# Kernel optimization log

Measured on AMD Instinct MI355X. Metric: run time of the kernel, lower is better.

The kernel has to match this reference:

```python
import jax, jax.numpy as jnp
import numpy as np

H = 16          # num_attention_heads
GRID = 16       # crop_size // patch_size
TOK_PER_FRAME = GRID * GRID


def _rope(x, pos, dim):
    # x: (B,H,N,dim), pos: (N,) int positions
    half = dim // 2
    omega = jnp.arange(half, dtype=x.dtype) / (dim / 2.0)
    inv = 1.0 / (10000.0 ** omega)                      # (half,)
    freq = pos.astype(x.dtype)[:, None] * inv            # (N, half)
    sin = jnp.concatenate([jnp.sin(freq), jnp.sin(freq)], axis=-1)  # (N, dim)  (tile, per source)
    cos = jnp.concatenate([jnp.cos(freq), jnp.cos(freq)], axis=-1)
    y = x.reshape(*x.shape[:-1], half, 2)
    y1, y2 = y[..., 0], y[..., 1]
    rot = jnp.stack((-y2, y1), axis=-1).reshape(x.shape)  # interleaved rotate-pairs
    return x * cos + rot * sin


def _apply_3d_rope(qk, f_ids, h_ids, w_ids, d_dim):
    s = 0
    parts = []
    for pos in (f_ids, h_ids, w_ids):
        parts.append(_rope(qk[..., s:s + d_dim], pos, d_dim))
        s += d_dim
    if s < qk.shape[-1]:
        parts.append(qk[..., s:])
    return jnp.concatenate(parts, axis=-1)


def setup_inputs() -> dict:
    key = jax.random.key(0)
    ks = jax.random.split(key, 5)
    D = 1024
    B, N = 4, 2048
    sc = 0.02
    return {
        "hidden_states": jax.random.normal(ks[0], (B, N, D), jnp.float32),
        "Wq": jax.random.normal(ks[1], (D, D), jnp.float32) * sc,
        "bq": jnp.zeros((D,), jnp.float32),
        "Wk": jax.random.normal(ks[2], (D, D), jnp.float32) * sc,
        "bk": jnp.zeros((D,), jnp.float32),
        "Wv": jax.random.normal(ks[3], (D, D), jnp.float32) * sc,
        "bv": jnp.zeros((D,), jnp.float32),
        "Wo": jax.random.normal(ks[4], (D, D), jnp.float32) * sc,
        "bo": jnp.zeros((D,), jnp.float32),
    }


def reference(hidden_states, Wq, bq, Wk, bk, Wv, bv, Wo, bo):
    B, N, D = hidden_states.shape
    hd = D // H
    d_dim = 2 * (hd // 3 // 2)  # per-component rotary dim (20 for hd=64)

    def heads(x):  # (B,N,D) -> (B,H,N,hd)
        return x.reshape(B, N, H, hd).transpose(0, 2, 1, 3)

    q = heads(hidden_states @ Wq + bq)
    k = heads(hidden_states @ Wk + bk)
    v = heads(hidden_states @ Wv + bv)

    ids = jnp.arange(N)
    f_ids = ids // TOK_PER_FRAME
    rem = ids - TOK_PER_FRAME * f_ids
    h_ids = rem // GRID
    w_ids = rem - GRID * h_ids

    q = _apply_3d_rope(q, f_ids, h_ids, w_ids, d_dim)
    k = _apply_3d_rope(k, f_ids, h_ids, w_ids, d_dim)

    scale = hd ** -0.5
    attn = jnp.einsum('bhqd,bhkd->bhqk', q, k) * scale
    attn = jax.nn.softmax(attn.astype(jnp.float32), axis=-1).astype(q.dtype)
    ctx = jnp.einsum('bhqk,bhkd->bhqd', attn, v)
    ctx = ctx.transpose(0, 2, 1, 3).reshape(B, N, D)
    return ctx @ Wo + bo
```

## Files before the change

### kernel.cpp

```cpp
#include <hip/hip_runtime.h>
#include <stdint.h>

#define H_   16
#define NS_  2048
#define B_   4
#define DM_  1024
#define HD_  64
#define MTOT (B_*NS_)

typedef __attribute__((ext_vector_type(8)))  short bf16x8;
typedef __attribute__((ext_vector_type(4)))  float f32x4;
typedef __attribute__((ext_vector_type(16))) float f32x16;

__device__ __forceinline__ unsigned short f2bf(float f){
  union { float f; unsigned u; } v; v.f = f;
  unsigned r = v.u + 0x7FFFu + ((v.u >> 16) & 1u);
  return (unsigned short)(r >> 16);
}
__device__ __forceinline__ float bf2f(unsigned short u){
  union { unsigned u; float f; } v; v.u = ((unsigned)u) << 16;
  return v.f;
}
__device__ __forceinline__ unsigned pk2(float a, float b){
  return (unsigned)f2bf(a) | ((unsigned)f2bf(b) << 16);
}
__device__ __forceinline__ unsigned cvtpk(float a, float b){
  unsigned r;
  asm("v_cvt_pk_bf16_f32 %0, %1, %2" : "=v"(r) : "v"(a), "v"(b));
  return r;
}
__device__ __forceinline__ float exp2a(float x){
  float r;
  asm("v_exp_f32 %0, %1" : "=v"(r) : "v"(x));
  return r;
}
__device__ __forceinline__ void gll16(const void* g, void* l){
  __builtin_amdgcn_global_load_lds(
      (const __attribute__((address_space(1))) unsigned int*)g,
      (__attribute__((address_space(3))) unsigned int*)l,
      16, 0, 0);
}

__global__ void k_cast_x(const float* __restrict__ x, unsigned short* __restrict__ xb){
  long i = ((long)blockIdx.x*256 + threadIdx.x)*4;
  float4 v = *(const float4*)(x + i);
  ushort4 o; o.x=f2bf(v.x); o.y=f2bf(v.y); o.z=f2bf(v.z); o.w=f2bf(v.w);
  *(ushort4*)(xb + i) = o;
}

__global__ void k_wt4(const float* __restrict__ W0, const float* __restrict__ W1,
                      const float* __restrict__ W2, const float* __restrict__ W3,
                      unsigned short* __restrict__ T0, unsigned short* __restrict__ T1,
                      unsigned short* __restrict__ T2, unsigned short* __restrict__ T3){
  __shared__ float tile[64][65];
  const int z = blockIdx.z;
  const float* W = (z==0)? W0 : (z==1)? W1 : (z==2)? W2 : W3;
  unsigned short* Wt = (z==0)? T0 : (z==1)? T1 : (z==2)? T2 : T3;
  int kt = blockIdx.y*64, nt = blockIdx.x*64;
  int t = threadIdx.x;
  int r = t >> 4, c4 = (t & 15)*4;
#pragma unroll
  for (int i=0;i<4;i++){
    int k = r + i*16;
    float4 v = *(const float4*)(W + (size_t)(kt + k)*DM_ + nt + c4);
    tile[k][c4] = v.x; tile[k][c4+1]=v.y; tile[k][c4+2]=v.z; tile[k][c4+3]=v.w;
  }
  __syncthreads();
#pragma unroll
  for (int i=0;i<4;i++){
    int n = r + i*16;
    ushort4 o;
    o.x = f2bf(tile[c4+0][n]); o.y = f2bf(tile[c4+1][n]);
    o.z = f2bf(tile[c4+2][n]); o.w = f2bf(tile[c4+3][n]);
    *(ushort4*)(Wt + (size_t)(nt + n)*DM_ + kt + c4) = o;
  }
}

__global__ void k_tab(float2* __restrict__ tab){
  int n = blockIdx.x*64 + threadIdx.x;
  int f = n >> 8, rem = n & 255, hh = rem >> 4, ww = rem & 15;
  float pos[3]; pos[0]=(float)f; pos[1]=(float)hh; pos[2]=(float)ww;
#pragma unroll
  for (int c=0;c<3;c++)
#pragma unroll
    for (int i=0;i<10;i++){
      float inv = exp2f(-(float)i * 1.3287712379549449f);
      float s, co;
      sincosf(pos[c]*inv, &s, &co);
      tab[n*30 + c*10 + i] = make_float2(co, s);
    }
}

__device__ __forceinline__ void stage256(const unsigned short* __restrict__ gsrc,
                                         char* ldst, int tid){
  const int srow = tid >> 3;
  const int gch  = (tid & 7) ^ (srow & 7);
  const unsigned short* gp = gsrc + (size_t)srow*DM_ + gch*8;
  char* lp = ldst + tid*16;
#pragma unroll
  for (int j=0;j<4;j++)
    gll16(gp + (size_t)(j*64)*DM_, lp + j*8192);
}

template<int MODE>
__global__ __launch_bounds__(512, 2) void k_gemm256(
    const unsigned short* __restrict__ A,
    const unsigned short* __restrict__ w0,
    const unsigned short* __restrict__ w1,
    const unsigned short* __restrict__ w2,
    const float* __restrict__ b0,
    const float* __restrict__ b1,
    const float* __restrict__ b2,
    unsigned short* __restrict__ Qb,
    unsigned short* __restrict__ Kb,
    unsigned short* __restrict__ VTb,
    float* __restrict__ Fout)
{
  extern __shared__ char smem[];
  char* aL = smem;
  char* bL = smem + 65536;
  const int tid = threadIdx.x, lane = tid & 63, w = tid >> 6;
  const int qc = lane & 15, g = lane >> 4;
  const int wm = (w >> 2)*128, wn = (w & 3)*64;

  int mat, mt, nt;
  {
    int id = blockIdx.x;
    if (MODE == 0){
      int wg = (id & 7)*48 + (id >> 3);
      mat = wg >> 7; int rem = wg & 127;
      mt = (rem >> 2)*256; nt = (rem & 3)*256;
    } else {
      int wg = (id & 7)*16 + (id >> 3);
      mat = 0; mt = (wg >> 2)*256; nt = (wg & 3)*256;
    }
  }
  const unsigned short* Wt = (MODE==1)? w0 : ((mat==0)? w0 : (mat==1)? w1 : w2);
  const float* bias        = (MODE==1)? b0 : ((mat==0)? b0 : (mat==1)? b1 : b2);

  const unsigned short* Ab = A  + (size_t)mt*DM_;
  const unsigned short* Bb = Wt + (size_t)nt*DM_;

  stage256(Ab,      aL,         tid);
  stage256(Bb,      bL,         tid);
  stage256(Ab + 64, aL + 32768, tid);
  stage256(Bb + 64, bL + 32768, tid);

  f32x4 acc[8][4] = {};

  for (int kt = 0; kt < 16; ++kt){
    const int bu = kt & 1;
    if (kt < 15) asm volatile("s_waitcnt vmcnt(8)" ::: "memory");
    else         asm volatile("s_waitcnt vmcnt(0)" ::: "memory");
    __builtin_amdgcn_s_barrier();
    __builtin_amdgcn_sched_barrier(0);
    const char* aT = aL + bu*32768;
    const char* bT = bL + bu*32768;

    bf16x8 bfr[4][2], af[4][2], af2[4][2];
#pragma unroll
    for (int n=0;n<4;n++)
#pragma unroll
      for (int ks=0;ks<2;ks++){
        int row = wn + n*16 + qc;
        bfr[n][ks] = *(const bf16x8*)(bT + row*128 + ((ks*64 + g*16) ^ ((row&7)<<4)));
      }
#pragma unroll
    for (int m=0;m<4;m++)
#pragma unroll
      for (int ks=0;ks<2;ks++){
        int row = wm + m*16 + qc;
        af[m][ks] = *(const bf16x8*)(aT + row*128 + ((ks*64 + g*16) ^ ((row&7)<<4)));
      }
    __builtin_amdgcn_s_setprio(1);
#pragma unroll
    for (int m=0;m<4;m++)
#pragma unroll
      for (int n=0;n<4;n++)
#pragma unroll
        for (int ks=0;ks<2;ks++)
          acc[m][n] = __builtin_amdgcn_mfma_f32_16x16x32_bf16(af[m][ks], bfr[n][ks], acc[m][n], 0,0,0);
    __builtin_amdgcn_s_setprio(0);
#pragma unroll
    for (int m=0;m<4;m++)
#pragma unroll
      for (int ks=0;ks<2;ks++){
        int row = wm + 64 + m*16 + qc;
        af2[m][ks] = *(const bf16x8*)(aT + row*128 + ((ks*64 + g*16) ^ ((row&7)<<4)));
      }
    asm volatile("s_waitcnt lgkmcnt(0)" ::: "memory");
    __builtin_amdgcn_sched_barrier(0);
    __builtin_amdgcn_s_barrier();
    __builtin_amdgcn_sched_barrier(0);
    if (kt < 14){
      stage256(Ab + (size_t)(kt+2)*64, aL + bu*32768, tid);
      stage256(Bb + (size_t)(kt+2)*64, bL + bu*32768, tid);
    }
    __builtin_amdgcn_s_setprio(1);
#pragma unroll
    for (int m=0;m<4;m++)
#pragma unroll
      for (int n=0;n<4;n++)
#pragma unroll
        for (int ks=0;ks<2;ks++)
          acc[4+m][n] = __builtin_amdgcn_mfma_f32_16x16x32_bf16(af2[m][ks], bfr[n][ks], acc[4+m][n], 0,0,0);
    __builtin_amdgcn_s_setprio(0);
  }

  if (MODE == 1){
#pragma unroll
    for (int n=0;n<4;n++){
      int col = nt + wn + n*16 + qc;
      float bv = bias[col];
#pragma unroll
      for (int m=0;m<8;m++){
#pragma unroll
        for (int r=0;r<4;r++){
          int mrow = mt + wm + m*16 + g*4 + r;
          Fout[(size_t)mrow*DM_ + col] = acc[m][n][r] + bv;
        }
      }
    }
  } else if (mat < 2){
    unsigned short* out = (mat==0)? Qb : Kb;
#pragma unroll
    for (int n=0;n<4;n++){
      int col = nt + wn + n*16 + qc;
      float bv = bias[col];
      int hh = col >> 6, d = col & 63;
#pragma unroll
      for (int m=0;m<8;m++){
#pragma unroll
        for (int r=0;r<4;r++){
          int mrow = mt + wm + m*16 + g*4 + r;
          size_t idx = (((size_t)(mrow >> 11)*H_ + hh)*NS_ + (mrow & (NS_-1)))*HD_ + d;
          out[idx] = f2bf(acc[m][n][r] + bv);
        }
      }
    }
  } else {
#pragma unroll
    for (int n=0;n<4;n++){
      int col = nt + wn + n*16 + qc;
      float bv = bias[col];
      int hh = col >> 6, d = col & 63;
#pragma unroll
      for (int m=0;m<8;m++){
        int mrow0 = mt + wm + m*16 + g*4;
        int b = mrow0 >> 11, ntk = mrow0 & (NS_-1);
        int pos = (ntk & ~12) | ((ntk & 4) << 1) | ((ntk & 8) >> 1);
        ushort4 o;
        o.x = f2bf(acc[m][n][0] + bv);
        o.y = f2bf(acc[m][n][1] + bv);
        o.z = f2bf(acc[m][n][2] + bv);
        o.w = f2bf(acc[m][n][3] + bv);
        *(ushort4*)(VTb + (((size_t)(b*H_ + hh)*HD_ + d)*NS_ + pos)) = o;
      }
    }
  }
}

#define QSCALE 0.18033688011112042f
__global__ void k_rope(unsigned short* __restrict__ Qb, unsigned short* __restrict__ Kb,
                       const float2* __restrict__ tab)
{
  const int t = threadIdx.x;
  const int d4 = (t & 15)*4;
  const long gtok = (long)blockIdx.x*16 + (t >> 4);
  size_t base = (size_t)gtok*HD_ + d4;
  if (d4 >= 60){
    ushort4 v = *(ushort4*)(Qb + base);
    ushort4 o;
    o.x = f2bf(bf2f(v.x)*QSCALE); o.y = f2bf(bf2f(v.y)*QSCALE);
    o.z = f2bf(bf2f(v.z)*QSCALE); o.w = f2bf(bf2f(v.w)*QSCALE);
    *(ushort4*)(Qb + base) = o;
    return;
  }
  const int n = (int)(gtok & (NS_-1));
  const int c = d4 / 20;
  const int dd = d4 - c*20;
  const float2* tb = tab + n*30 + c*10;
  float2 cs0 = tb[(dd+0) % 10];
  float2 cs1 = tb[(dd+1) % 10];
  float2 cs2 = tb[(dd+2) % 10];
  float2 cs3 = tb[(dd+3) % 10];
#pragma unroll
  for (int which = 0; which < 2; which++){
    unsigned short* P = which ? Kb : Qb;
    float sc = which ? 1.f : QSCALE;
    ushort4 v = *(ushort4*)(P + base);
    float x0=bf2f(v.x), x1=bf2f(v.y), x2=bf2f(v.z), x3=bf2f(v.w);
    ushort4 o;
    o.x = f2bf((x0*cs0.x - x1*cs0.y)*sc);
    o.y = f2bf((x1*cs1.x + x0*cs1.y)*sc);
    o.z = f2bf((x2*cs2.x - x3*cs2.y)*sc);
    o.w = f2bf((x3*cs3.x + x2*cs3.y)*sc);
    *(ushort4*)(P + base) = o;
  }
}

__global__ __launch_bounds__(256, 4) void k_attn(const unsigned short* __restrict__ Q,
                                                 const unsigned short* __restrict__ K,
                                                 const unsigned short* __restrict__ VT,
                                                 unsigned short* __restrict__ ctxout)
{
  __shared__ __attribute__((aligned(16))) char smem[32768];
  const int tid  = threadIdx.x;
  const int lane = tid & 63, w = tid >> 6;
  const int qcol = lane & 31, h = lane >> 5;
  const int sw   = (lane & 7) << 4;
  const int bh   = blockIdx.x;
  const int q0   = blockIdx.y*128 + w*32;

  const unsigned short* Qp = Q  + ((size_t)bh*NS_ + q0)*HD_;
  const unsigned short* Kp = K  + (size_t)bh*NS_*HD_;
  const unsigned short* Vp = VT + (size_t)bh*HD_*NS_;

  const int trow = tid >> 3;
  const int tc   = (tid & 7) ^ (trow & 7);

  bf16x8 qf[4];
#pragma unroll
  for (int i=0;i<4;i++)
    qf[i] = *(const bf16x8*)(Qp + (size_t)qcol*HD_ + 16*i + 8*h);

  {
    const unsigned short* gk = Kp + (size_t)trow*HD_ + tc*8;
    const unsigned short* gv = Vp + (size_t)trow*NS_ + tc*8;
    gll16(gk,          smem + w*1024);
    gll16(gk + 32*HD_, smem + 4096 + w*1024);
    gll16(gv,          smem + 8192 + w*1024);
    gll16(gv + 32*NS_, smem + 8192 + 4096 + w*1024);
  }

  f32x16 ctx0 = {}, ctx1 = {};
  float mrun = -1e30f, lp = 0.f;

  for (int t = 0; t < NS_/64; ++t){
    const int curo = (t & 1) * 16384;
    __syncthreads();
    if (t + 1 < NS_/64){
      const int kb = (t+1)*64;
      const int nxt = ((t+1) & 1) * 16384;
      const unsigned short* gk = Kp + (size_t)(kb + trow)*HD_ + tc*8;
      const unsigned short* gv = Vp + (size_t)trow*NS_ + kb + tc*8;
      gll16(gk,          smem + nxt + w*1024);
      gll16(gk + 32*HD_, smem + nxt + 4096 + w*1024);
      gll16(gv,          smem + nxt + 8192 + w*1024);
      gll16(gv + 32*NS_, smem + nxt + 8192 + 4096 + w*1024);
    }
    const char* kls = smem + curo;
    const char* vls = smem + curo + 8192;

#pragma unroll
    for (int s = 0; s < 2; ++s){
      f32x16 st = {};
      __builtin_amdgcn_s_setprio(1);
#pragma unroll
      for (int i=0;i<4;i++){
        bf16x8 kf = *(const bf16x8*)(kls + ((((32*s + qcol)*128) + 32*i + 16*h) ^ sw));
        st = __builtin_amdgcn_mfma_f32_32x32x16_bf16(kf, qf[i], st, 0,0,0);
      }
      __builtin_amdgcn_s_setprio(0);
      float a0 = fmaxf(fmaxf(st[0],  st[1]),  st[2]);
      float a1 = fmaxf(fmaxf(st[3],  st[4]),  st[5]);
      float a2 = fmaxf(fmaxf(st[6],  st[7]),  st[8]);
      float a3 = fmaxf(fmaxf(st[9],  st[10]), st[11]);
      float a4 = fmaxf(fmaxf(st[12], st[13]), st[14]);
      float tm = fmaxf(fmaxf(fmaxf(a0,a1),a2), fmaxf(fmaxf(a3,a4),st[15]));
      if (!__all(tm - mrun <= 11.5f)){
        float tp = fmaxf(tm, __shfl_xor(tm, 32));
        float mnew = fmaxf(mrun, tp);
        float alpha = exp2a(mrun - mnew);
        lp *= alpha;
#pragma unroll
        for (int r=0;r<16;r++){ ctx0[r]*=alpha; ctx1[r]*=alpha; }
        mrun = mnew;
      }
      unsigned u[8];
      float ps = 0.f;
#pragma unroll
      for (int r=0;r<8;r++){
        float ea = exp2a(st[2*r]   - mrun);
        float eb = exp2a(st[2*r+1] - mrun);
        unsigned uu = cvtpk(ea, eb);
        u[r] = uu;
        union { unsigned q; float f; } lo, hi;
        lo.q = uu << 16; hi.q = uu & 0xFFFF0000u;
        ps += lo.f + hi.f;
      }
      lp += ps;
      bf16x8 pf0 = __builtin_bit_cast(bf16x8, make_uint4(u[0],u[1],u[2],u[3]));
      bf16x8 pf1 = __builtin_bit_cast(bf16x8, make_uint4(u[4],u[5],u[6],u[7]));

      __builtin_amdgcn_s_setprio(1);
#pragma unroll
      for (int kc=0; kc<2; ++kc){
        const bf16x8 pf = kc ? pf1 : pf0;
        bf16x8 vf0 = *(const bf16x8*)(vls + ((qcol)*128      + ((64*s + 32*kc + 16*h) ^ sw)));
        ctx0 = __builtin_amdgcn_mfma_f32_32x32x16_bf16(vf0, pf, ctx0, 0,0,0);
        bf16x8 vf1 = *(const bf16x8*)(vls + ((32 + qcol)*128 + ((64*s + 32*kc + 16*h) ^ sw)));
        ctx1 = __builtin_amdgcn_mfma_f32_32x32x16_bf16(vf1, pf, ctx1, 0,0,0);
      }
      __builtin_amdgcn_s_setprio(0);
    }
  }

  float lsum = lp + __shfl_xor(lp, 32);
  float linv = 1.f / lsum;
  __syncthreads();
  char* reg = smem + w*4096;
#pragma unroll
  for (int rq=0; rq<4; ++rq){
    int db0 = 8*rq + 4*h;
    uint2 v0, v1;
    v0.x = pk2(ctx0[4*rq+0]*linv, ctx0[4*rq+1]*linv);
    v0.y = pk2(ctx0[4*rq+2]*linv, ctx0[4*rq+3]*linv);
    v1.x = pk2(ctx1[4*rq+0]*linv, ctx1[4*rq+1]*linv);
    v1.y = pk2(ctx1[4*rq+2]*linv, ctx1[4*rq+3]*linv);
    *(uint2*)(reg + qcol*128 + db0*2)      = v0;
    *(uint2*)(reg + qcol*128 + (32+db0)*2) = v1;
  }
  __syncthreads();
  const int b = bh >> 4, head = bh & 15;
  unsigned short* outp = ctxout + ((size_t)b*NS_ + q0)*DM_ + head*HD_;
#pragma unroll
  for (int p=0;p<4;p++){
    int row = p*8 + (lane>>3);
    uint4 v = *(const uint4*)(reg + row*128 + (lane&7)*16);
    *(uint4*)(outp + (size_t)row*DM_ + (lane&7)*8) = v;
  }
}

extern "C" void kernel_launch(void* const* d_in, const int* in_sizes, int n_in,
                              void* d_out, int out_size, void* d_ws, size_t ws_size,
                              hipStream_t stream)
{
  const float* hs = (const float*)d_in[0];
  const float* Wq = (const float*)d_in[1];
  const float* bq = (const float*)d_in[2];
  const float* Wk = (const float*)d_in[3];
  const float* bk = (const float*)d_in[4];
  const float* Wv = (const float*)d_in[5];
  const float* bv = (const float*)d_in[6];
  const float* Wo = (const float*)d_in[7];
  const float* bo = (const float*)d_in[8];

  char* ws = (char*)d_ws;
  size_t off = 0;
  auto alloc = [&](size_t b){ void* p = ws + off; off += (b + 255) & ~(size_t)255; return p; };
  unsigned short* xb  = (unsigned short*)alloc((size_t)MTOT*DM_*2);
  unsigned short* wqt = (unsigned short*)alloc((size_t)DM_*DM_*2);
  unsigned short* wkt = (unsigned short*)alloc((size_t)DM_*DM_*2);
  unsigned short* wvt = (unsigned short*)alloc((size_t)DM_*DM_*2);
  unsigned short* wot = (unsigned short*)alloc((size_t)DM_*DM_*2);
  float2*         tab = (float2*)alloc((size_t)NS_*30*sizeof(float2));
  unsigned short* Qb  = (unsigned short*)alloc((size_t)MTOT*DM_*2);
  unsigned short* Kb  = (unsigned short*)alloc((size_t)MTOT*DM_*2);
  unsigned short* VTb = (unsigned short*)alloc((size_t)MTOT*DM_*2);
  unsigned short* cxb = (unsigned short*)alloc((size_t)MTOT*DM_*2);

  hipFuncSetAttribute((const void*)k_gemm256<0>,
                      hipFuncAttributeMaxDynamicSharedMemorySize, 131072);
  hipFuncSetAttribute((const void*)k_gemm256<1>,
                      hipFuncAttributeMaxDynamicSharedMemorySize, 131072);

  k_cast_x<<<dim3(MTOT*DM_/1024), dim3(256), 0, stream>>>(hs, xb);
  k_wt4<<<dim3(16,16,4), dim3(256), 0, stream>>>(Wq, Wk, Wv, Wo, wqt, wkt, wvt, wot);
  k_tab<<<dim3(32), dim3(64), 0, stream>>>(tab);

  k_gemm256<0><<<dim3(384), dim3(512), 131072, stream>>>(
      xb, wqt, wkt, wvt, bq, bk, bv, Qb, Kb, VTb, (float*)nullptr);

  k_rope<<<dim3(64*NS_/16), dim3(256), 0, stream>>>(Qb, Kb, tab);

  k_attn<<<dim3(64, 16), dim3(256), 0, stream>>>(Qb, Kb, VTb, cxb);

  k_gemm256<1><<<dim3(128), dim3(512), 131072, stream>>>(
      cxb, wot, nullptr, nullptr, bo, nullptr, nullptr,
      nullptr, nullptr, nullptr, (float*)d_out);
}
```

Baseline: 240.0 us.

## Merge prep kernels, store Q/K token-major, restructure rope and attention QK

Folds the x cast, weight transposes and rope-table kernels into a single launch with block-range dispatch, removing two launches. The QKV GEMM now writes Q and K in plain (B,N,D) row-major order instead of a head-major scatter, so the epilogue stores stay coalesced along columns. The rope kernel and the attention loads are updated for the row stride of DM_, and rope handles 8 elements per thread. In attention, both 32-row QK^T MFMA tiles are issued before the softmax to give the scheduler more overlap. In exchange, attention K loads become strided across rows of 1024 elements, which may hurt load efficiency.

```diff
diff --git a/kernel.cpp b/kernel.cpp
--- a/kernel.cpp
+++ b/kernel.cpp
@@ -41,54 +41,60 @@
       16, 0, 0);
 }
 
-__global__ void k_cast_x(const float* __restrict__ x, unsigned short* __restrict__ xb){
-  long i = ((long)blockIdx.x*256 + threadIdx.x)*4;
-  float4 v = *(const float4*)(x + i);
-  ushort4 o; o.x=f2bf(v.x); o.y=f2bf(v.y); o.z=f2bf(v.z); o.w=f2bf(v.w);
-  *(ushort4*)(xb + i) = o;
-}
-
-__global__ void k_wt4(const float* __restrict__ W0, const float* __restrict__ W1,
-                      const float* __restrict__ W2, const float* __restrict__ W3,
-                      unsigned short* __restrict__ T0, unsigned short* __restrict__ T1,
-                      unsigned short* __restrict__ T2, unsigned short* __restrict__ T3){
+__global__ void k_prep(const float* __restrict__ hs, unsigned short* __restrict__ xb,
+                       const float* __restrict__ W0, const float* __restrict__ W1,
+                       const float* __restrict__ W2, const float* __restrict__ W3,
+                       unsigned short* __restrict__ T0, unsigned short* __restrict__ T1,
+                       unsigned short* __restrict__ T2, unsigned short* __restrict__ T3,
+                       float2* __restrict__ tab)
+{
   __shared__ float tile[64][65];
-  const int z = blockIdx.z;
-  const float* W = (z==0)? W0 : (z==1)? W1 : (z==2)? W2 : W3;
-  unsigned short* Wt = (z==0)? T0 : (z==1)? T1 : (z==2)? T2 : T3;
-  int kt = blockIdx.y*64, nt = blockIdx.x*64;
-  int t = threadIdx.x;
-  int r = t >> 4, c4 = (t & 15)*4;
-#pragma unroll
-  for (int i=0;i<4;i++){
-    int k = r + i*16;
-    float4 v = *(const float4*)(W + (size_t)(kt + k)*DM_ + nt + c4);
-    tile[k][c4] = v.x; tile[k][c4+1]=v.y; tile[k][c4+2]=v.z; tile[k][c4+3]=v.w;
-  }
-  __syncthreads();
-#pragma unroll
-  for (int i=0;i<4;i++){
-    int n = r + i*16;
-    ushort4 o;
-    o.x = f2bf(tile[c4+0][n]); o.y = f2bf(tile[c4+1][n]);
-    o.z = f2bf(tile[c4+2][n]); o.w = f2bf(tile[c4+3][n]);
-    *(ushort4*)(Wt + (size_t)(nt + n)*DM_ + kt + c4) = o;
-  }
-}
-
-__global__ void k_tab(float2* __restrict__ tab){
-  int n = blockIdx.x*64 + threadIdx.x;
-  int f = n >> 8, rem = n & 255, hh = rem >> 4, ww = rem & 15;
-  float pos[3]; pos[0]=(float)f; pos[1]=(float)hh; pos[2]=(float)ww;
-#pragma unroll
-  for (int c=0;c<3;c++)
-#pragma unroll
-    for (int i=0;i<10;i++){
-      float inv = exp2f(-(float)i * 1.3287712379549449f);
-      float s, co;
-      sincosf(pos[c]*inv, &s, &co);
-      tab[n*30 + c*10 + i] = make_float2(co, s);
-    }
+  const int bid = blockIdx.x, t = threadIdx.x;
+  if (bid < 8192){
+    long i = ((long)bid*256 + t)*4;
+    float4 v = *(const float4*)(hs + i);
+    ushort4 o; o.x=f2bf(v.x); o.y=f2bf(v.y); o.z=f2bf(v.z); o.w=f2bf(v.w);
+    *(ushort4*)(xb + i) = o;
+    return;
+  }
+  if (bid < 9216){
+    int id = bid - 8192;
+    const int z = id >> 8; id &= 255;
+    const float* W = (z==0)? W0 : (z==1)? W1 : (z==2)? W2 : W3;
+    unsigned short* Wt = (z==0)? T0 : (z==1)? T1 : (z==2)? T2 : T3;
+    int kt = (id >> 4)*64, nt = (id & 15)*64;
+    int r = t >> 4, c4 = (t & 15)*4;
+#pragma unroll
+    for (int i=0;i<4;i++){
+      int k = r + i*16;
+      float4 v = *(const float4*)(W + (size_t)(kt + k)*DM_ + nt + c4);
+      tile[k][c4] = v.x; tile[k][c4+1]=v.y; tile[k][c4+2]=v.z; tile[k][c4+3]=v.w;
+    }
+    __syncthreads();
+#pragma unroll
+    for (int i=0;i<4;i++){
+      int n = r + i*16;
+      ushort4 o;
+      o.x = f2bf(tile[c4+0][n]); o.y = f2bf(tile[c4+1][n]);
+      o.z = f2bf(tile[c4+2][n]); o.w = f2bf(tile[c4+3][n]);
+      *(ushort4*)(Wt + (size_t)(nt + n)*DM_ + kt + c4) = o;
+    }
+    return;
+  }
+  {
+    int n = (bid - 9216)*256 + t;
+    int f = n >> 8, rem = n & 255, hh = rem >> 4, ww = rem & 15;
+    float pos[3]; pos[0]=(float)f; pos[1]=(float)hh; pos[2]=(float)ww;
+#pragma unroll
+    for (int c=0;c<3;c++)
+#pragma unroll
+      for (int i=0;i<10;i++){
+        float inv = exp2f(-(float)i * 1.3287712379549449f);
+        float s, co;
+        sincosf(pos[c]*inv, &s, &co);
+        tab[n*30 + c*10 + i] = make_float2(co, s);
+      }
+  }
 }
 
 __device__ __forceinline__ void stage256(const unsigned short* __restrict__ gsrc,
@@ -227,14 +233,12 @@
     for (int n=0;n<4;n++){
       int col = nt + wn + n*16 + qc;
       float bv = bias[col];
-      int hh = col >> 6, d = col & 63;
 #pragma unroll
       for (int m=0;m<8;m++){
 #pragma unroll
         for (int r=0;r<4;r++){
           int mrow = mt + wm + m*16 + g*4 + r;
-          size_t idx = (((size_t)(mrow >> 11)*H_ + hh)*NS_ + (mrow & (NS_-1)))*HD_ + d;
-          out[idx] = f2bf(acc[m][n][r] + bv);
+          out[(size_t)mrow*DM_ + col] = f2bf(acc[m][n][r] + bv);
         }
       }
     }
@@ -265,37 +269,38 @@
                        const float2* __restrict__ tab)
 {
   const int t = threadIdx.x;
-  const int d4 = (t & 15)*4;
-  const long gtok = (long)blockIdx.x*16 + (t >> 4);
-  size_t base = (size_t)gtok*HD_ + d4;
-  if (d4 >= 60){
-    ushort4 v = *(ushort4*)(Qb + base);
-    ushort4 o;
-    o.x = f2bf(bf2f(v.x)*QSCALE); o.y = f2bf(bf2f(v.y)*QSCALE);
-    o.z = f2bf(bf2f(v.z)*QSCALE); o.w = f2bf(bf2f(v.w)*QSCALE);
-    *(ushort4*)(Qb + base) = o;
-    return;
-  }
-  const int n = (int)(gtok & (NS_-1));
-  const int c = d4 / 20;
-  const int dd = d4 - c*20;
-  const float2* tb = tab + n*30 + c*10;
-  float2 cs0 = tb[(dd+0) % 10];
-  float2 cs1 = tb[(dd+1) % 10];
-  float2 cs2 = tb[(dd+2) % 10];
-  float2 cs3 = tb[(dd+3) % 10];
+  const long token = (long)blockIdx.x*2 + (t >> 7);
+  const int fd = (t & 127)*8;
+  const int n = (int)(token & (NS_-1));
+  const int d = fd & 63;
+  const float2* tb = tab + n*30;
+  float2 cs[8];
+#pragma unroll
+  for (int j=0;j<8;j++){
+    int e = d + j;
+    if (e < 60){
+      int c = e/20; int rr = e - 20*c; if (rr >= 10) rr -= 10;
+      cs[j] = tb[c*10 + rr];
+    } else cs[j] = make_float2(1.f, 0.f);
+  }
+  size_t base = (size_t)token*DM_ + fd;
 #pragma unroll
   for (int which = 0; which < 2; which++){
     unsigned short* P = which ? Kb : Qb;
     float sc = which ? 1.f : QSCALE;
-    ushort4 v = *(ushort4*)(P + base);
-    float x0=bf2f(v.x), x1=bf2f(v.y), x2=bf2f(v.z), x3=bf2f(v.w);
-    ushort4 o;
-    o.x = f2bf((x0*cs0.x - x1*cs0.y)*sc);
-    o.y = f2bf((x1*cs1.x + x0*cs1.y)*sc);
-    o.z = f2bf((x2*cs2.x - x3*cs2.y)*sc);
-    o.w = f2bf((x3*cs3.x + x2*cs3.y)*sc);
-    *(ushort4*)(P + base) = o;
+    ushort4 va = *(ushort4*)(P + base);
+    ushort4 vb = *(ushort4*)(P + base + 4);
+    float x[8] = {bf2f(va.x),bf2f(va.y),bf2f(va.z),bf2f(va.w),
+                  bf2f(vb.x),bf2f(vb.y),bf2f(vb.z),bf2f(vb.w)};
+    unsigned short o[8];
+#pragma unroll
+    for (int j=0;j<8;j+=2){
+      o[j]   = f2bf((x[j]*cs[j].x     - x[j+1]*cs[j].y)  *sc);
+      o[j+1] = f2bf((x[j+1]*cs[j+1].x + x[j]*cs[j+1].y)  *sc);
+    }
+    ushort4 oa = {o[0],o[1],o[2],o[3]}, ob = {o[4],o[5],o[6],o[7]};
+    *(ushort4*)(P + base)     = oa;
+    *(ushort4*)(P + base + 4) = ob;
   }
 }
 
@@ -310,10 +315,11 @@
   const int qcol = lane & 31, h = lane >> 5;
   const int sw   = (lane & 7) << 4;
   const int bh   = blockIdx.x;
+  const int b    = bh >> 4, head = bh & 15;
   const int q0   = blockIdx.y*128 + w*32;
 
-  const unsigned short* Qp = Q  + ((size_t)bh*NS_ + q0)*HD_;
-  const unsigned short* Kp = K  + (size_t)bh*NS_*HD_;
+  const unsigned short* Qp = Q  + ((size_t)(b*NS_ + q0))*DM_ + head*HD_;
+  const unsigned short* Kp = K  + ((size_t)(b*NS_))*DM_ + head*HD_;
   const unsigned short* Vp = VT + (size_t)bh*HD_*NS_;
 
   const int trow = tid >> 3;
@@ -322,13 +328,13 @@
   bf16x8 qf[4];
 #pragma unroll
   for (int i=0;i<4;i++)
-    qf[i] = *(const bf16x8*)(Qp + (size_t)qcol*HD_ + 16*i + 8*h);
+    qf[i] = *(const bf16x8*)(Qp + (size_t)qcol*DM_ + 16*i + 8*h);
 
   {
-    const unsigned short* gk = Kp + (size_t)trow*HD_ + tc*8;
+    const unsigned short* gk = Kp + (size_t)trow*DM_ + tc*8;
     const unsigned short* gv = Vp + (size_t)trow*NS_ + tc*8;
     gll16(gk,          smem + w*1024);
-    gll16(gk + 32*HD_, smem + 4096 + w*1024);
+    gll16(gk + 32*DM_, smem + 4096 + w*1024);
     gll16(gv,          smem + 8192 + w*1024);
     gll16(gv + 32*NS_, smem + 8192 + 4096 + w*1024);
   }
@@ -342,26 +348,33 @@
     if (t + 1 < NS_/64){
       const int kb = (t+1)*64;
       const int nxt = ((t+1) & 1) * 16384;
-      const unsigned short* gk = Kp + (size_t)(kb + trow)*HD_ + tc*8;
+      const unsigned short* gk = Kp + (size_t)(kb + trow)*DM_ + tc*8;
       const unsigned short* gv = Vp + (size_t)trow*NS_ + kb + tc*8;
       gll16(gk,          smem + nxt + w*1024);
-      gll16(gk + 32*HD_, smem + nxt + 4096 + w*1024);
+      gll16(gk + 32*DM_, smem + nxt + 4096 + w*1024);
       gll16(gv,          smem + nxt + 8192 + w*1024);
       gll16(gv + 32*NS_, smem + nxt + 8192 + 4096 + w*1024);
     }
     const char* kls = smem + curo;
     const char* vls = smem + curo + 8192;
 
+    f32x16 st0 = {}, st1 = {};
+    __builtin_amdgcn_s_setprio(1);
+#pragma unroll
+    for (int i=0;i<4;i++){
+      bf16x8 kf = *(const bf16x8*)(kls + (((qcol)*128 + 32*i + 16*h) ^ sw));
+      st0 = __builtin_amdgcn_mfma_f32_32x32x16_bf16(kf, qf[i], st0, 0,0,0);
+    }
+#pragma unroll
+    for (int i=0;i<4;i++){
+      bf16x8 kf = *(const bf16x8*)(kls + ((((32 + qcol)*128) + 32*i + 16*h) ^ sw));
+      st1 = __builtin_amdgcn_mfma_f32_32x32x16_bf16(kf, qf[i], st1, 0,0,0);
+    }
+    __builtin_amdgcn_s_setprio(0);
+
 #pragma unroll
     for (int s = 0; s < 2; ++s){
-      f32x16 st = {};
-      __builtin_amdgcn_s_setprio(1);
-#pragma unroll
-      for (int i=0;i<4;i++){
-        bf16x8 kf = *(const bf16x8*)(kls + ((((32*s + qcol)*128) + 32*i + 16*h) ^ sw));
-        st = __builtin_amdgcn_mfma_f32_32x32x16_bf16(kf, qf[i], st, 0,0,0);
-      }
-      __builtin_amdgcn_s_setprio(0);
+      f32x16& st = s ? st1 : st0;
       float a0 = fmaxf(fmaxf(st[0],  st[1]),  st[2]);
       float a1 = fmaxf(fmaxf(st[3],  st[4]),  st[5]);
       float a2 = fmaxf(fmaxf(st[6],  st[7]),  st[8]);
@@ -422,8 +435,7 @@
     *(uint2*)(reg + qcol*128 + (32+db0)*2) = v1;
   }
   __syncthreads();
-  const int b = bh >> 4, head = bh & 15;
-  unsigned short* outp = ctxout + ((size_t)b*NS_ + q0)*DM_ + head*HD_;
+  unsigned short* outp = ctxout + ((size_t)(b*NS_ + q0))*DM_ + head*HD_;
 #pragma unroll
   for (int p=0;p<4;p++){
     int row = p*8 + (lane>>3);
@@ -465,14 +477,13 @@
   hipFuncSetAttribute((const void*)k_gemm256<1>,
                       hipFuncAttributeMaxDynamicSharedMemorySize, 131072);
 
-  k_cast_x<<<dim3(MTOT*DM_/1024), dim3(256), 0, stream>>>(hs, xb);
-  k_wt4<<<dim3(16,16,4), dim3(256), 0, stream>>>(Wq, Wk, Wv, Wo, wqt, wkt, wvt, wot);
-  k_tab<<<dim3(32), dim3(64), 0, stream>>>(tab);
+  k_prep<<<dim3(9224), dim3(256), 0, stream>>>(hs, xb, Wq, Wk, Wv, Wo,
+                                               wqt, wkt, wvt, wot, tab);
 
   k_gemm256<0><<<dim3(384), dim3(512), 131072, stream>>>(
       xb, wqt, wkt, wvt, bq, bk, bv, Qb, Kb, VTb, (float*)nullptr);
 
-  k_rope<<<dim3(64*NS_/16), dim3(256), 0, stream>>>(Qb, Kb, tab);
+  k_rope<<<dim3(MTOT/2), dim3(256), 0, stream>>>(Qb, Kb, tab);
 
   k_attn<<<dim3(64, 16), dim3(256), 0, stream>>>(Qb, Kb, VTb, cxb);
 
```

Result: no change. 235.5 us (-1.9%).
